# Kernel tuning notes

Measured on AMD Instinct MI355X. Metric: run time of the kernel, lower is better.

The kernel has to match this reference:

```python
import jax, jax.numpy as jnp
import numpy as np
from jax import lax

N, E, DIN, D, L, H, T, NE = 20000, 240000, 768, 256, 3, 4, 9, 8  # nodes, edges, input_dim, gnn_dim, layers, heads, tags, n_etype
DH = D // H
BN_EPS = 1e-5

def _bn(x, g, b):
    # eval-mode BatchNorm1d with running stats (mean=0, var=1)
    return x * (g / np.sqrt(1.0 + BN_EPS)) + b

def _gelu(x):
    return jax.nn.gelu(x, approximate=False)

def setup_inputs():
    key = jax.random.key(0)
    ks = iter(jax.random.split(key, 48))
    nrm = lambda shape: jax.random.normal(next(ks), shape, jnp.float32) * 0.02
    return {
        "node_emb": jax.random.normal(next(ks), (N, DIN), jnp.float32),
        "edge_index": jax.random.randint(next(ks), (2, E), 0, N),
        "edge_type": jax.random.randint(next(ks), (E,), 0, NE),
        "tag_gt": jax.random.randint(next(ks), (N,), 0, T),
        "W_lm2gnn": nrm((DIN, D)), "b_lm2gnn": jnp.zeros((D,)),
        "We1": nrm((L, NE + 1, D)), "be1": jnp.zeros((L, D)),
        "g1": jnp.ones((L, D)), "bb1": jnp.zeros((L, D)),
        "We2": nrm((L, D, D)), "be2": jnp.zeros((L, D)),
        "Wq": nrm((L, D, D)), "bq": jnp.zeros((L, D)),
        "Wk": nrm((L, 2 * D, D)), "bk": jnp.zeros((L, D)),
        "Wm": nrm((L, 2 * D, D)), "bm": jnp.zeros((L, D)),
        "Wp1": nrm((L, D, D)), "bp1": jnp.zeros((L, D)),
        "g2": jnp.ones((L, D)), "bb2": jnp.zeros((L, D)),
        "Wp2": nrm((L, D, D)), "bp2": jnp.zeros((L, D)),
        "Wo": nrm((D, D)), "bo": jnp.zeros((D,)),
        "Wc": nrm((D, D)), "bc": jnp.zeros((D,)),
        "Wt": nrm((D, T)), "bt": jnp.zeros((T,)),
        "crf_start": nrm((T,)), "crf_end": nrm((T,)), "crf_trans": nrm((T, T)),
    }

def _emissions(node_emb, edge_index, edge_type, W_lm2gnn, b_lm2gnn, We1, be1, g1, bb1,
               We2, be2, Wq, bq, Wk, bk, Wm, bm, Wp1, bp1, g2, bb2, Wp2, bp2,
               Wo, bo, Wc, bc, Wt, bt):
    H0 = _gelu(node_emb @ W_lm2gnn + b_lm2gnn)
    loop = jnp.arange(N)
    src = jnp.concatenate([edge_index[0], loop])          # (Etot,)
    dst = jnp.concatenate([edge_index[1], loop])
    # one-hot edge types + self-loop type NE
    ev = jnp.concatenate([jax.nn.one_hot(edge_type, NE + 1, dtype=jnp.float32),
                          jnp.zeros((N, NE + 1), jnp.float32).at[:, NE].set(1.0)], axis=0)
    deg = jax.ops.segment_sum(jnp.ones_like(src, jnp.float32), src, N)[src]  # src out-degree per edge
    X = H0
    for l in range(L):
        e = _bn(ev @ We1[l] + be1[l], g1[l], bb1[l])
        e = jax.nn.relu(e) @ We2[l] + be2[l]              # edge embeddings (Etot, D)
        x_i, x_j = X[dst], X[src]                          # target, source gathers
        q = (x_j @ Wq[l] + bq[l]).reshape(-1, H, DH)
        k = (x_i @ Wk[l][:D] + e @ Wk[l][D:] + bk[l]).reshape(-1, H, DH)
        m = (x_j @ Wm[l][:D] + e @ Wm[l][D:] + bm[l]).reshape(-1, H, DH)
        s = (q * k).sum(-1) / np.sqrt(DH)                  # (Etot, H)
        smax = jax.ops.segment_max(s, src, N)[src]
        ex = jnp.exp(s - smax)
        den = jax.ops.segment_sum(ex, src, N)[src]
        alpha = ex / (den + 1e-16) * deg[:, None]          # segment softmax over src, degree-scaled
        out_e = (m * alpha[:, :, None]).reshape(-1, D)
        aggr = jax.ops.segment_sum(out_e, dst, N)          # scatter-add to targets
        Xl = _bn(aggr @ Wp1[l] + bp1[l], g2[l], bb2[l])
        X = _gelu(jax.nn.relu(Xl) @ Wp2[l] + bp2[l])       # mlp then activation (dropout = eval identity)
    hidden = _gelu((H0 @ Wo + bo) + (X @ Wc + bc))
    return hidden @ Wt + bt                                # (N, T)

def reference(node_emb, edge_index, edge_type, tag_gt, W_lm2gnn, b_lm2gnn, We1, be1, g1, bb1,
              We2, be2, Wq, bq, Wk, bk, Wm, bm, Wp1, bp1, g2, bb2, Wp2, bp2,
              Wo, bo, Wc, bc, Wt, bt, crf_start, crf_end, crf_trans):
    em = _emissions(node_emb, edge_index, edge_type, W_lm2gnn, b_lm2gnn, We1, be1, g1, bb1,
                    We2, be2, Wq, bq, Wk, bk, Wm, bm, Wp1, bp1, g2, bb2, Wp2, bp2,
                    Wo, bo, Wc, bc, Wt, bt)
    # CRF Viterbi decode (batch=1, full-length mask)
    def vstep(score, em_t):
        cand = score[:, None] + crf_trans                  # (T, T)
        return jnp.max(cand, axis=0) + em_t, jnp.argmax(cand, axis=0)
    last, bps = lax.scan(vstep, crf_start + em[0], em[1:])
    last_tag = jnp.argmax(last + crf_end)
    def back(t, bp_t):
        prev = bp_t[t]
        return prev, prev
    _, prevs = lax.scan(back, last_tag, bps, reverse=True)
    path = jnp.concatenate([prevs, last_tag[None]])
    return path[None, :]                                   # (1, N) best tag sequence
```

## Files before the change

kernel.cpp:

```cpp
#include <hip/hip_runtime.h>

#define NN 20000
#define EE 240000
#define ETOTAL 260000
#define DIN 768
#define DD 256
#define NT 9

typedef __attribute__((ext_vector_type(2))) float f32x2;

__device__ __forceinline__ unsigned fenc(float x) {
  unsigned u = __float_as_uint(x);
  return (u & 0x80000000u) ? ~u : (u | 0x80000000u);
}
__device__ __forceinline__ float fdec(unsigned e) {
  unsigned u = (e & 0x80000000u) ? (e ^ 0x80000000u) : ~e;
  return __uint_as_float(u);
}
__device__ __forceinline__ float gelu_f(float x) {
  return 0.5f * x * (1.0f + erff(x * 0.70710678118654752440f));
}

#define VSTEP_CORE(EIN, SIN, SOUT)                                        \
  asm volatile(                                                           \
    "s_nop 2\n\t"                                                         \
    "v_readlane_b32 s84, %[sv], 0\n\t"                                    \
    "v_readlane_b32 s85, %[sv], 1\n\t"                                    \
    "v_readlane_b32 s86, %[sv], 2\n\t"                                    \
    "v_readlane_b32 s87, %[sv], 3\n\t"                                    \
    "v_readlane_b32 s88, %[sv], 4\n\t"                                    \
    "v_readlane_b32 s89, %[sv], 5\n\t"                                    \
    "v_readlane_b32 s90, %[sv], 6\n\t"                                    \
    "v_readlane_b32 s91, %[sv], 7\n\t"                                    \
    "v_readlane_b32 s92, %[sv], 8\n\t"                                    \
    "v_pk_add_f32 v[80:81], s[84:85], %[u01]\n\t"                         \
    "v_pk_add_f32 v[82:83], s[86:87], %[u23]\n\t"                         \
    "v_pk_add_f32 v[84:85], s[88:89], %[u45]\n\t"                         \
    "v_pk_add_f32 v[86:87], s[90:91], %[u67]\n\t"                         \
    "v_add_f32 v88, s92, %[u8]\n\t"                                       \
    "v_max3_f32 v80, v80, v81, v82\n\t"                                   \
    "v_max3_f32 v83, v83, v84, v85\n\t"                                   \
    "v_max3_f32 v86, v86, v87, v88\n\t"                                   \
    "v_max3_f32 v80, v80, v83, v86\n\t"                                   \
    "v_add_f32 %[out], v80, %[e]\n\t"                                     \
    : [out]"=v"(SOUT)                                                     \
    : [sv]"v"(SIN), [e]"v"(EIN),                                          \
      [u01]"v"(tc01), [u23]"v"(tc23), [u45]"v"(tc45), [u67]"v"(tc67),     \
      [u8]"v"(tcol8)                                                      \
    : "s84","s85","s86","s87","s88","s89","s90","s91","s92",              \
      "v80","v81","v82","v83","v84","v85","v86","v87","v88")

#define RUN8(E0, E1) do {                                                 \
  float s0, s1, s2, s3, s4, s5, s6, s7;                                   \
  VSTEP_CORE((E0).x, s, s0); VSTEP_CORE((E0).y, s0, s1);                  \
  VSTEP_CORE((E0).z, s1, s2); VSTEP_CORE((E0).w, s2, s3);                 \
  float4 stq0; stq0.x = s0; stq0.y = s1; stq0.z = s2; stq0.w = s3;        \
  *(float4*)svp = stq0;                                                   \
  VSTEP_CORE((E1).x, s3, s4); VSTEP_CORE((E1).y, s4, s5);                 \
  VSTEP_CORE((E1).z, s5, s6); VSTEP_CORE((E1).w, s6, s7);                 \
  float4 stq1; stq1.x = s4; stq1.y = s5; stq1.z = s6; stq1.w = s7;        \
  *(float4*)(svp + 256) = stq1;                                           \
  s = s7; svp += 512;                                                     \
} while (0)

__global__ __launch_bounds__(256) void gemm_k(
    const float* __restrict__ A, const float* __restrict__ B,
    const float* __restrict__ bias,
    const float* __restrict__ bng, const float* __restrict__ bnb,
    float* __restrict__ C, int M, int K, int N, int act)
{
  __shared__ float As[32][64];
  __shared__ float Bs[32][64];
  const int tid = threadIdx.x;
  const int tx = tid & 15, ty = tid >> 4;
  const int m0 = blockIdx.y * 64, n0 = blockIdx.x * 64;
  float acc[4][4];
#pragma unroll
  for (int i = 0; i < 4; ++i)
#pragma unroll
    for (int j = 0; j < 4; ++j) acc[i][j] = 0.f;

  for (int kk = 0; kk < K; kk += 32) {
#pragma unroll
    for (int L = tid; L < 512; L += 256) {
      int r = L >> 3, c4 = L & 7;
      int gm = m0 + r;
      float4 v = make_float4(0.f, 0.f, 0.f, 0.f);
      if (gm < M) v = *(const float4*)(A + (size_t)gm * K + kk + c4 * 4);
      As[c4 * 4 + 0][r] = v.x; As[c4 * 4 + 1][r] = v.y;
      As[c4 * 4 + 2][r] = v.z; As[c4 * 4 + 3][r] = v.w;
    }
#pragma unroll
    for (int L = tid; L < 512; L += 256) {
      int r = L >> 4, c4 = L & 15;
      *(float4*)&Bs[r][c4 * 4] = *(const float4*)(B + (size_t)(kk + r) * N + n0 + c4 * 4);
    }
    __syncthreads();
#pragma unroll
    for (int k = 0; k < 32; ++k) {
      float a[4], b[4];
      *(float4*)a = *(const float4*)&As[k][ty * 4];
      *(float4*)b = *(const float4*)&Bs[k][tx * 4];
#pragma unroll
      for (int i = 0; i < 4; ++i)
#pragma unroll
        for (int j = 0; j < 4; ++j) acc[i][j] += a[i] * b[j];
    }
    __syncthreads();
  }
  const float bnc = 0.99999500003749968752f;
#pragma unroll
  for (int i = 0; i < 4; ++i) {
    int gm = m0 + ty * 4 + i;
    if (gm >= M) continue;
    float o[4];
#pragma unroll
    for (int j = 0; j < 4; ++j) {
      int n = n0 + tx * 4 + j;
      float x = acc[i][j];
      if (bias) x += bias[n];
      if (act == 1) x = gelu_f(x);
      else if (act == 2) { x = x * (bng[n] * bnc) + bnb[n]; x = fmaxf(x, 0.f); }
      o[j] = x;
    }
    *(float4*)(C + (size_t)gm * N + n0 + tx * 4) = *(const float4*)o;
  }
}

__global__ __launch_bounds__(256) void gemm3_k(
    const float* __restrict__ A, const float* __restrict__ B0,
    const float* __restrict__ bias0, const float* __restrict__ B1,
    const float* __restrict__ B2, float* __restrict__ C0,
    float* __restrict__ C1, float* __restrict__ C2, int M)
{
  __shared__ float As[32][64];
  __shared__ float Bs[3][32][64];
  const int tid = threadIdx.x;
  const int tx = tid & 15, ty = tid >> 4;
  const int m0 = blockIdx.y * 64, n0 = blockIdx.x * 64;
  float acc0[4][4], acc1[4][4], acc2[4][4];
#pragma unroll
  for (int i = 0; i < 4; ++i)
#pragma unroll
    for (int j = 0; j < 4; ++j) { acc0[i][j] = 0.f; acc1[i][j] = 0.f; acc2[i][j] = 0.f; }

  for (int kk = 0; kk < DD; kk += 32) {
#pragma unroll
    for (int L = tid; L < 512; L += 256) {
      int r = L >> 3, c4 = L & 7;
      int gm = m0 + r;
      float4 v = make_float4(0.f, 0.f, 0.f, 0.f);
      if (gm < M) v = *(const float4*)(A + (size_t)gm * DD + kk + c4 * 4);
      As[c4 * 4 + 0][r] = v.x; As[c4 * 4 + 1][r] = v.y;
      As[c4 * 4 + 2][r] = v.z; As[c4 * 4 + 3][r] = v.w;
    }
#pragma unroll
    for (int L = tid; L < 1536; L += 256) {
      int which = L >> 9, r = (L >> 4) & 31, c4 = L & 15;
      const float* Bp = (which == 0) ? B0 : (which == 1) ? B1 : B2;
      *(float4*)&Bs[which][r][c4 * 4] =
          *(const float4*)(Bp + (size_t)(kk + r) * DD + n0 + c4 * 4);
    }
    __syncthreads();
#pragma unroll
    for (int k = 0; k < 32; ++k) {
      float a[4], b0[4], b1[4], b2[4];
      *(float4*)a = *(const float4*)&As[k][ty * 4];
      *(float4*)b0 = *(const float4*)&Bs[0][k][tx * 4];
      *(float4*)b1 = *(const float4*)&Bs[1][k][tx * 4];
      *(float4*)b2 = *(const float4*)&Bs[2][k][tx * 4];
#pragma unroll
      for (int i = 0; i < 4; ++i)
#pragma unroll
        for (int j = 0; j < 4; ++j) {
          acc0[i][j] += a[i] * b0[j];
          acc1[i][j] += a[i] * b1[j];
          acc2[i][j] += a[i] * b2[j];
        }
    }
    __syncthreads();
  }
#pragma unroll
  for (int i = 0; i < 4; ++i) {
    int gm = m0 + ty * 4 + i;
    if (gm >= M) continue;
    float o0[4], o1[4], o2[4];
#pragma unroll
    for (int j = 0; j < 4; ++j) {
      int n = n0 + tx * 4 + j;
      o0[j] = acc0[i][j] + bias0[n];
      o1[j] = acc1[i][j];
      o2[j] = acc2[i][j];
    }
    *(float4*)(C0 + (size_t)gm * DD + n0 + tx * 4) = *(const float4*)o0;
    *(float4*)(C1 + (size_t)gm * DD + n0 + tx * 4) = *(const float4*)o1;
    *(float4*)(C2 + (size_t)gm * DD + n0 + tx * 4) = *(const float4*)o2;
  }
}

__global__ __launch_bounds__(256) void gemm_cat_k(
    const float* __restrict__ A1, const float* __restrict__ B1,
    const float* __restrict__ bias1, const float* __restrict__ A2,
    const float* __restrict__ B2, const float* __restrict__ bias2,
    float* __restrict__ C, int M)
{
  __shared__ float As[32][64];
  __shared__ float Bs[32][64];
  const int tid = threadIdx.x;
  const int tx = tid & 15, ty = tid >> 4;
  const int m0 = blockIdx.y * 64, n0 = blockIdx.x * 64;
  float acc[4][4];
#pragma unroll
  for (int i = 0; i < 4; ++i)
#pragma unroll
    for (int j = 0; j < 4; ++j) acc[i][j] = 0.f;

  for (int kk = 0; kk < 2 * DD; kk += 32) {
    const float* Ap = (kk < DD) ? A1 : A2;
    const float* Bp = (kk < DD) ? B1 : B2;
    const int ko = kk & (DD - 1);
#pragma unroll
    for (int L = tid; L < 512; L += 256) {
      int r = L >> 3, c4 = L & 7;
      int gm = m0 + r;
      float4 v = make_float4(0.f, 0.f, 0.f, 0.f);
      if (gm < M) v = *(const float4*)(Ap + (size_t)gm * DD + ko + c4 * 4);
      As[c4 * 4 + 0][r] = v.x; As[c4 * 4 + 1][r] = v.y;
      As[c4 * 4 + 2][r] = v.z; As[c4 * 4 + 3][r] = v.w;
    }
#pragma unroll
    for (int L = tid; L < 512; L += 256) {
      int r = L >> 4, c4 = L & 15;
      *(float4*)&Bs[r][c4 * 4] = *(const float4*)(Bp + (size_t)(ko + r) * DD + n0 + c4 * 4);
    }
    __syncthreads();
#pragma unroll
    for (int k = 0; k < 32; ++k) {
      float a[4], b[4];
      *(float4*)a = *(const float4*)&As[k][ty * 4];
      *(float4*)b = *(const float4*)&Bs[k][tx * 4];
#pragma unroll
      for (int i = 0; i < 4; ++i)
#pragma unroll
        for (int j = 0; j < 4; ++j) acc[i][j] += a[i] * b[j];
    }
    __syncthreads();
  }
#pragma unroll
  for (int i = 0; i < 4; ++i) {
    int gm = m0 + ty * 4 + i;
    if (gm >= M) continue;
    float o[4];
#pragma unroll
    for (int j = 0; j < 4; ++j) {
      int n = n0 + tx * 4 + j;
      o[j] = gelu_f(acc[i][j] + bias1[n] + bias2[n]);
    }
    *(float4*)(C + (size_t)gm * DD + n0 + tx * 4) = *(const float4*)o;
  }
}

__global__ __launch_bounds__(256) void edge_tables_k(
    const float* __restrict__ We1l, const float* __restrict__ be1l,
    const float* __restrict__ g1l, const float* __restrict__ bb1l,
    const float* __restrict__ We2l, const float* __restrict__ be2l,
    const float* __restrict__ WkEl, const float* __restrict__ bkl,
    const float* __restrict__ WmEl, const float* __restrict__ bml,
    float* __restrict__ ketab, float* __restrict__ metab)
{
  __shared__ float r_s[DD];
  __shared__ float e_s[DD];
  const int t = blockIdx.x, d = threadIdx.x;
  const float bnc = 0.99999500003749968752f;
  float pre = We1l[t * DD + d] + be1l[d];
  float bnv = pre * (g1l[d] * bnc) + bb1l[d];
  r_s[d] = fmaxf(bnv, 0.f);
  __syncthreads();
  float acc = 0.f;
  for (int c = 0; c < DD; ++c) acc += r_s[c] * We2l[c * DD + d];
  e_s[d] = acc + be2l[d];
  __syncthreads();
  float ka = 0.f, ma = 0.f;
  for (int c = 0; c < DD; ++c) {
    float ec = e_s[c];
    ka += ec * WkEl[c * DD + d];
    ma += ec * WmEl[c * DD + d];
  }
  ketab[t * DD + d] = ka + bkl[d];
  metab[t * DD + d] = ma + bml[d];
}

__global__ void deg_k(const int* __restrict__ ei, int* __restrict__ cnt,
                      int* __restrict__ cnt_d)
{
  for (int e = blockIdx.x * blockDim.x + threadIdx.x; e < EE; e += gridDim.x * blockDim.x) {
    atomicAdd(&cnt[ei[e]], 1);
    atomicAdd(&cnt_d[ei[EE + e]], 1);
  }
}

__global__ __launch_bounds__(256) void scan_k(const int* __restrict__ c,
                                              int* __restrict__ offs)
{
  __shared__ int part[257];
  const int tid = threadIdx.x;
  const int CH = (NN + 255) / 256;
  int a = tid * CH, b = a + CH; if (b > NN) b = NN;
  int s = 0;
  for (int i = a; i < b; ++i) s += c[i];
  part[tid] = s;
  __syncthreads();
  if (tid == 0) {
    int r = 0;
    for (int i = 0; i < 256; ++i) { int v = part[i]; part[i] = r; r += v; }
    part[256] = r;
  }
  __syncthreads();
  int r = part[tid];
  for (int i = a; i < b; ++i) { offs[i] = r; r += c[i]; }
  if (tid == 255) offs[NN] = part[256];
}

__global__ void fill_k(const int* __restrict__ ei, const int* __restrict__ offs,
                       int* __restrict__ fc, int* __restrict__ eix)
{
  for (int e = blockIdx.x * blockDim.x + threadIdx.x; e < EE; e += gridDim.x * blockDim.x) {
    int d = ei[EE + e];
    int p = offs[d] + atomicAdd(&fc[d], 1);
    eix[p] = e;
  }
}

__global__ __launch_bounds__(256) void score_k(
    const float* __restrict__ Q, const float* __restrict__ Kn,
    const float* __restrict__ ketab, const int* __restrict__ ei,
    const int* __restrict__ et, float* __restrict__ sbuf,
    unsigned* __restrict__ smax)
{
  __shared__ float ke_s[NT * DD];
  for (int i = threadIdx.x; i < NT * DD; i += 256) ke_s[i] = ketab[i];
  __syncthreads();
  const int lane = threadIdx.x & 63, wave = threadIdx.x >> 6;
  const float4* Q4 = (const float4*)Q;
  const float4* K4 = (const float4*)Kn;
  for (int e = blockIdx.x * 4 + wave; e < ETOTAL; e += gridDim.x * 4) {
    int src, dst, t;
    if (e < EE) { src = ei[e]; dst = ei[EE + e]; t = et[e]; }
    else { src = dst = e - EE; t = NT - 1; }
    float4 q = Q4[src * 64 + lane];
    float4 k = K4[dst * 64 + lane];
    float4 ke = *(const float4*)(ke_s + t * DD + lane * 4);
    float p = q.x * (k.x + ke.x) + q.y * (k.y + ke.y) +
              q.z * (k.z + ke.z) + q.w * (k.w + ke.w);
    p += __shfl_xor(p, 8); p += __shfl_xor(p, 4);
    p += __shfl_xor(p, 2); p += __shfl_xor(p, 1);
    if ((lane & 15) == 0) {
      int h = lane >> 4;
      float s = p * 0.125f;
      sbuf[e * 4 + h] = s;
      atomicMax(smax + src * 4 + h, fenc(s));
    }
  }
}

__global__ void softmax_k(const int* __restrict__ ei, float* __restrict__ sbuf,
                          const unsigned* __restrict__ smax, float* __restrict__ den)
{
  for (int idx = blockIdx.x * blockDim.x + threadIdx.x; idx < ETOTAL * 4;
       idx += gridDim.x * blockDim.x) {
    int e = idx >> 2, h = idx & 3;
    int src = (e < EE) ? ei[e] : e - EE;
    float s = sbuf[idx];
    float ex = expf(s - fdec(smax[src * 4 + h]));
    sbuf[idx] = ex;
    atomicAdd(den + src * 4 + h, ex);
  }
}

__global__ __launch_bounds__(256) void aggr2_k(
    const float* __restrict__ Mn, const float* __restrict__ metab,
    const int* __restrict__ ei, const int* __restrict__ et,
    const float* __restrict__ sbuf, const float* __restrict__ den,
    const int* __restrict__ cnt, const int* __restrict__ offs,
    const int* __restrict__ eix, float* __restrict__ aggr)
{
  __shared__ float me_s[NT * DD];
  for (int i = threadIdx.x; i < NT * DD; i += 256) me_s[i] = metab[i];
  __syncthreads();
  const int lane = threadIdx.x & 63, wave = threadIdx.x >> 6;
  const int h = lane >> 4;
  const float4* M4 = (const float4*)Mn;
  int dst = blockIdx.x * 4 + wave;
  if (dst >= NN) return;
  float4 acc;
  {
    float ex = sbuf[(EE + dst) * 4 + h];
    float dn = den[dst * 4 + h];
    float alpha = ex / (dn + 1e-16f) * (float)(cnt[dst] + 1);
    float4 m = M4[dst * 64 + lane];
    float4 me = *(const float4*)(me_s + (NT - 1) * DD + lane * 4);
    acc.x = (m.x + me.x) * alpha; acc.y = (m.y + me.y) * alpha;
    acc.z = (m.z + me.z) * alpha; acc.w = (m.w + me.w) * alpha;
  }
  int o1 = offs[dst + 1];
  for (int o = offs[dst]; o < o1; ++o) {
    int e = eix[o];
    int src = ei[e], t = et[e];
    float ex = sbuf[e * 4 + h];
    float dn = den[src * 4 + h];
    float alpha = ex / (dn + 1e-16f) * (float)(cnt[src] + 1);
    float4 m = M4[src * 64 + lane];
    float4 me = *(const float4*)(me_s + t * DD + lane * 4);
    acc.x += (m.x + me.x) * alpha; acc.y += (m.y + me.y) * alpha;
    acc.z += (m.z + me.z) * alpha; acc.w += (m.w + me.w) * alpha;
  }
  ((float4*)aggr)[dst * 64 + lane] = acc;
}

__global__ __launch_bounds__(256) void emis_k(
    const float* __restrict__ hidden, const float* __restrict__ Wt,
    const float* __restrict__ bt, float* __restrict__ em)
{
  __shared__ float wt_s[DD * NT];
  for (int i = threadIdx.x; i < DD * NT; i += 256) wt_s[i] = Wt[i];
  __syncthreads();
  const int lane = threadIdx.x & 63, wave = threadIdx.x >> 6;
  const float4* H4 = (const float4*)hidden;
  for (int n = blockIdx.x * 4 + wave; n < NN; n += gridDim.x * 4) {
    float4 h = H4[n * 64 + lane];
    const float* w0 = wt_s + (lane * 4) * NT;
    float p[NT];
#pragma unroll
    for (int t = 0; t < NT; ++t)
      p[t] = h.x * w0[t] + h.y * w0[NT + t] + h.z * w0[2 * NT + t] + h.w * w0[3 * NT + t];
#pragma unroll
    for (int m = 32; m >= 1; m >>= 1)
#pragma unroll
      for (int t = 0; t < NT; ++t) p[t] += __shfl_xor(p[t], m);
    if (lane == 0) {
#pragma unroll
      for (int t = 0; t < NT; ++t) em[n * NT + t] = p[t] + bt[t];
    }
  }
}

__global__ __launch_bounds__(256) void viterbi_k(
    const float* __restrict__ em, const float* __restrict__ cstart,
    const float* __restrict__ cend, const float* __restrict__ ctrans,
    float* __restrict__ sv, int* __restrict__ outp)
{
  const int VCS = 512;
  const int ST = VCS + 12;
  const int NCH = (NN + VCS - 1) / VCS;
  __shared__ float embufT[2][NT][VCS + 12];
  __shared__ float trT[NT * 16];
  __shared__ float scf[NT];
  __shared__ unsigned char fmaps[256][NT];
  __shared__ unsigned char ends_s[256];
  __shared__ int last_s;
  const int tid = threadIdx.x, lane = tid & 63, wave = tid >> 6;
  const int jl = min(lane & 15, NT - 1);

  for (int i = tid; i < VCS * NT; i += 256) {
    int t = i / NT, j = i - t * NT;
    embufT[0][j][t] = em[i];
  }
  if (tid < NT * NT) trT[(tid % NT) * 16 + (tid / NT)] = ctrans[tid];
  __syncthreads();

  f32x2 tc01, tc23, tc45, tc67;
  float tcol8 = 0.f;
  float s = 0.f;
  if (wave == 0) {
    tc01[0] = ctrans[0 * NT + jl]; tc01[1] = ctrans[1 * NT + jl];
    tc23[0] = ctrans[2 * NT + jl]; tc23[1] = ctrans[3 * NT + jl];
    tc45[0] = ctrans[4 * NT + jl]; tc45[1] = ctrans[5 * NT + jl];
    tc67[0] = ctrans[6 * NT + jl]; tc67[1] = ctrans[7 * NT + jl];
    tcol8   = ctrans[8 * NT + jl];
    s = cstart[jl] + embufT[0][jl][0];
    sv[lane * 4] = s;
  }

  for (int c = 0; c < NCH; ++c) {
    if (wave > 0) {
      if (c + 1 < NCH) {
        int base = (c + 1) * VCS * NT;
        int n2 = VCS * NT;
        if (base + n2 > NN * NT) n2 = NN * NT - base;
        float* dstb = &embufT[(c + 1) & 1][0][0];
        for (int i = tid - 64; i < n2; i += 192) {
          int t = i / NT, j = i - t * NT;
          dstb[j * ST + t] = em[base + i];
        }
      }
    } else {
      const float* ebT = &embufT[c & 1][0][0] + (size_t)jl * ST;
      int tbeg = (c == 0) ? 1 : c * VCS;
      int tend = (c + 1) * VCS; if (tend > NN) tend = NN;
      int off = tbeg - c * VCS;
      int nsteps = tend - tbeg;
      int pre = (8 - (tbeg & 7)) & 7; if (pre > nsteps) pre = nsteps;
      for (int i = 0; i < pre; ++i) {
        int t = tbeg + i;
        float e0 = ebT[off + i];
        float so;
        VSTEP_CORE(e0, s, so);
        s = so;
        sv[((size_t)t >> 2) * 256 + lane * 4 + (t & 3)] = s;
      }
      int rem = nsteps - pre;
      int ngr = rem >> 3;
      int tof = off + pre;
      float* svp = sv + ((size_t)(tbeg + pre) >> 2) * 256 + lane * 4;
      if (ngr > 0) {
        float4 eA0 = *(const float4*)&ebT[tof];
        float4 eA1 = *(const float4*)&ebT[tof + 4];
        float4 eB0, eB1;
        int g = 0;
        while (g + 2 <= ngr) {
          eB0 = *(const float4*)&ebT[tof + (g + 1) * 8];
          eB1 = *(const float4*)&ebT[tof + (g + 1) * 8 + 4];
          RUN8(eA0, eA1);
          eA0 = *(const float4*)&ebT[tof + (g + 2) * 8];
          eA1 = *(const float4*)&ebT[tof + (g + 2) * 8 + 4];
          RUN8(eB0, eB1);
          g += 2;
        }
        if (g < ngr) RUN8(eA0, eA1);
      }
      for (int i = pre + (ngr << 3); i < nsteps; ++i) {
        int t = tbeg + i;
        float e0 = ebT[off + i];
        float so;
        VSTEP_CORE(e0, s, so);
        s = so;
        sv[((size_t)t >> 2) * 256 + lane * 4 + (t & 3)] = s;
      }
    }
    __syncthreads();
  }

  if (wave == 0 && lane < NT) scf[lane] = s + cend[lane];
  __syncthreads();
  if (tid == 0) {
    float bv = scf[0]; int bi = 0;
    for (int j = 1; j < NT; ++j) if (scf[j] > bv) { bv = scf[j]; bi = j; }
    last_s = bi;
  }
  __syncthreads();

  const int RL = 79;
  int a = 1 + tid * RL;
  int b = a + RL; if (b > NN) b = NN;
  bool active = (a < NN);
  if (active) {
    int x[NT];
#pragma unroll
    for (int j = 0; j < NT; ++j) x[j] = j;
    for (int t = b - 1; t >= a; --t) {
      const float* sp = sv + ((size_t)(t - 1) >> 2) * 256 + ((t - 1) & 3);
      float sr[NT];
#pragma unroll
      for (int i = 0; i < NT; ++i) sr[i] = sp[i * 4];
#pragma unroll
      for (int j = 0; j < NT; ++j) {
        const float* tcx = trT + x[j] * 16;
        float bv = sr[0] + tcx[0]; int bi = 0;
#pragma unroll
        for (int i = 1; i < NT; ++i) {
          float cv = sr[i] + tcx[i];
          if (cv > bv) { bv = cv; bi = i; }
        }
        x[j] = bi;
      }
    }
#pragma unroll
    for (int j = 0; j < NT; ++j) fmaps[tid][j] = (unsigned char)x[j];
  }
  __syncthreads();
  if (tid == 0) {
    int x = last_s;
    for (int k = 255; k >= 0; --k) {
      ends_s[k] = (unsigned char)x;
      int ak = 1 + k * RL;
      if (ak < NN) x = fmaps[k][x];
    }
  }
  __syncthreads();
  if (active) {
    int x = ends_s[tid];
    outp[b - 1] = x;
    for (int t = b - 1; t >= a; --t) {
      const float* sp = sv + ((size_t)(t - 1) >> 2) * 256 + ((t - 1) & 3);
      const float* tcx = trT + x * 16;
      float bv = sp[0] + tcx[0]; int bi = 0;
#pragma unroll
      for (int i = 1; i < NT; ++i) {
        float cv = sp[i * 4] + tcx[i];
        if (cv > bv) { bv = cv; bi = i; }
      }
      x = bi;
      outp[t - 1] = x;
    }
  }
}

extern "C" void kernel_launch(void* const* d_in, const int* in_sizes, int n_in,
                              void* d_out, int out_size, void* d_ws, size_t ws_size,
                              hipStream_t stream)
{
  const float* node_emb = (const float*)d_in[0];
  const int* edge_index = (const int*)d_in[1];
  const int* edge_type = (const int*)d_in[2];
  const float* W_lm2gnn = (const float*)d_in[4];
  const float* b_lm2gnn = (const float*)d_in[5];
  const float* We1 = (const float*)d_in[6];
  const float* be1 = (const float*)d_in[7];
  const float* g1 = (const float*)d_in[8];
  const float* bb1 = (const float*)d_in[9];
  const float* We2 = (const float*)d_in[10];
  const float* be2 = (const float*)d_in[11];
  const float* Wq = (const float*)d_in[12];
  const float* bq = (const float*)d_in[13];
  const float* Wk = (const float*)d_in[14];
  const float* bk = (const float*)d_in[15];
  const float* Wm = (const float*)d_in[16];
  const float* bm = (const float*)d_in[17];
  const float* Wp1 = (const float*)d_in[18];
  const float* bp1 = (const float*)d_in[19];
  const float* g2 = (const float*)d_in[20];
  const float* bb2 = (const float*)d_in[21];
  const float* Wp2 = (const float*)d_in[22];
  const float* bp2 = (const float*)d_in[23];
  const float* Wo = (const float*)d_in[24];
  const float* bo = (const float*)d_in[25];
  const float* Wc = (const float*)d_in[26];
  const float* bc = (const float*)d_in[27];
  const float* Wt = (const float*)d_in[28];
  const float* bt = (const float*)d_in[29];
  const float* cstart = (const float*)d_in[30];
  const float* cend = (const float*)d_in[31];
  const float* ctrans = (const float*)d_in[32];

  const size_t NB = (size_t)NN * DD * sizeof(float);
  char* w = (char*)d_ws;
  float* H0 = (float*)(w + 0 * NB);
  float* Xb = (float*)(w + 1 * NB);
  float* Qb = (float*)(w + 2 * NB);
  float* Kb = (float*)(w + 3 * NB);
  float* Mb = (float*)(w + 4 * NB);
  char* sm = w + 5 * NB;
  size_t smo = 0;
  auto alloc = [&](size_t bytes) { char* p = sm + smo; smo += (bytes + 255) & ~255ull; return p; };
  float* sbuf = (float*)alloc((size_t)ETOTAL * 4 * 4);
  unsigned* smax = (unsigned*)alloc((size_t)NN * 4 * 4);
  float* den = (float*)alloc((size_t)NN * 4 * 4);
  int* cnt = (int*)alloc((size_t)NN * 4);
  int* cnt_d = (int*)alloc((size_t)NN * 4);
  int* offs = (int*)alloc((size_t)(NN + 1) * 4);
  int* fc = (int*)alloc((size_t)NN * 4);
  int* eix = (int*)alloc((size_t)EE * 4);
  float* ketab = (float*)alloc((size_t)NT * DD * 4);
  float* metab = (float*)alloc((size_t)NT * DD * 4);
  float* em = (float*)alloc((size_t)NN * NT * 4);
  float* sv = (float*)alloc(((size_t)NN * 64 + 256) * 4);
  const size_t needed = 5 * NB + smo;
  if (ws_size < needed) return;

  dim3 gg(DD / 64, (NN + 63) / 64);

  hipMemsetAsync(cnt, 0, (size_t)((char*)eix - (char*)cnt), stream);
  deg_k<<<1024, 256, 0, stream>>>(edge_index, cnt, cnt_d);
  scan_k<<<1, 256, 0, stream>>>(cnt_d, offs);
  fill_k<<<1024, 256, 0, stream>>>(edge_index, offs, fc, eix);

  gemm_k<<<gg, 256, 0, stream>>>(node_emb, W_lm2gnn, b_lm2gnn, nullptr,
                                 nullptr, H0, NN, DIN, DD, 1);

  const float* Xcur = H0;
  for (int l = 0; l < 3; ++l) {
    edge_tables_k<<<NT, 256, 0, stream>>>(
        We1 + (size_t)l * NT * DD, be1 + l * DD, g1 + l * DD, bb1 + l * DD,
        We2 + (size_t)l * DD * DD, be2 + l * DD,
        Wk + (size_t)l * 2 * DD * DD + DD * DD, bk + l * DD,
        Wm + (size_t)l * 2 * DD * DD + DD * DD, bm + l * DD, ketab, metab);

    gemm3_k<<<gg, 256, 0, stream>>>(Xcur, Wq + (size_t)l * DD * DD, bq + l * DD,
                                    Wk + (size_t)l * 2 * DD * DD,
                                    Wm + (size_t)l * 2 * DD * DD,
                                    Qb, Kb, Mb, NN);

    hipMemsetAsync(smax, 0, (size_t)NN * 4 * 4 * 2, stream);
    score_k<<<2048, 256, 0, stream>>>(Qb, Kb, ketab, edge_index, edge_type, sbuf, smax);
    softmax_k<<<2048, 256, 0, stream>>>(edge_index, sbuf, smax, den);

    aggr2_k<<<(NN + 3) / 4, 256, 0, stream>>>(Mb, metab, edge_index, edge_type,
                                              sbuf, den, cnt, offs, eix, Kb);

    gemm_k<<<gg, 256, 0, stream>>>(Kb, Wp1 + (size_t)l * DD * DD, bp1 + l * DD,
                                   g2 + l * DD, bb2 + l * DD, Qb, NN, DD, DD, 2);
    gemm_k<<<gg, 256, 0, stream>>>(Qb, Wp2 + (size_t)l * DD * DD, bp2 + l * DD,
                                   nullptr, nullptr, Xb, NN, DD, DD, 1);
    Xcur = Xb;
  }

  gemm_cat_k<<<gg, 256, 0, stream>>>(H0, Wo, bo, Xb, Wc, bc, Qb, NN);

  emis_k<<<1250, 256, 0, stream>>>(Qb, Wt, bt, em);
  viterbi_k<<<1, 256, 0, stream>>>(em, cstart, cend, ctrans, sv, (int*)d_out);
}
```

Baseline: 2.719 ms.

## Replace atomic edge softmax with source-sorted CSR segmented softmax

Builds a second CSR index grouped by source node and computes each node's per-head softmax max and denominator with one wave per node using shuffle reductions. This replaces the atomicMax/atomicAdd scatter kernels and the per-layer memset. The exponential is now recomputed inside the aggregation kernel from the stored max and sum. The cost is an extra scan and fill pass at setup, plus more expf work and a float2 load in aggregation.

```diff
diff --git a/kernel.cpp b/kernel.cpp
--- a/kernel.cpp
+++ b/kernel.cpp
@@ -9,14 +9,6 @@
 
 typedef __attribute__((ext_vector_type(2))) float f32x2;
 
-__device__ __forceinline__ unsigned fenc(float x) {
-  unsigned u = __float_as_uint(x);
-  return (u & 0x80000000u) ? ~u : (u | 0x80000000u);
-}
-__device__ __forceinline__ float fdec(unsigned e) {
-  unsigned u = (e & 0x80000000u) ? (e ^ 0x80000000u) : ~e;
-  return __uint_as_float(u);
-}
 __device__ __forceinline__ float gelu_f(float x) {
   return 0.5f * x * (1.0f + erff(x * 0.70710678118654752440f));
 }
@@ -321,11 +313,11 @@
   if (tid == 255) offs[NN] = part[256];
 }
 
-__global__ void fill_k(const int* __restrict__ ei, const int* __restrict__ offs,
+__global__ void fill_k(const int* __restrict__ key, const int* __restrict__ offs,
                        int* __restrict__ fc, int* __restrict__ eix)
 {
   for (int e = blockIdx.x * blockDim.x + threadIdx.x; e < EE; e += gridDim.x * blockDim.x) {
-    int d = ei[EE + e];
+    int d = key[e];
     int p = offs[d] + atomicAdd(&fc[d], 1);
     eix[p] = e;
   }
@@ -334,8 +326,7 @@
 __global__ __launch_bounds__(256) void score_k(
     const float* __restrict__ Q, const float* __restrict__ Kn,
     const float* __restrict__ ketab, const int* __restrict__ ei,
-    const int* __restrict__ et, float* __restrict__ sbuf,
-    unsigned* __restrict__ smax)
+    const int* __restrict__ et, float* __restrict__ sbuf)
 {
   __shared__ float ke_s[NT * DD];
   for (int i = threadIdx.x; i < NT * DD; i += 256) ke_s[i] = ketab[i];
@@ -356,31 +347,42 @@
     p += __shfl_xor(p, 2); p += __shfl_xor(p, 1);
     if ((lane & 15) == 0) {
       int h = lane >> 4;
-      float s = p * 0.125f;
-      sbuf[e * 4 + h] = s;
-      atomicMax(smax + src * 4 + h, fenc(s));
-    }
-  }
-}
-
-__global__ void softmax_k(const int* __restrict__ ei, float* __restrict__ sbuf,
-                          const unsigned* __restrict__ smax, float* __restrict__ den)
-{
-  for (int idx = blockIdx.x * blockDim.x + threadIdx.x; idx < ETOTAL * 4;
-       idx += gridDim.x * blockDim.x) {
-    int e = idx >> 2, h = idx & 3;
-    int src = (e < EE) ? ei[e] : e - EE;
-    float s = sbuf[idx];
-    float ex = expf(s - fdec(smax[src * 4 + h]));
-    sbuf[idx] = ex;
-    atomicAdd(den + src * 4 + h, ex);
-  }
+      sbuf[e * 4 + h] = p * 0.125f;
+    }
+  }
+}
+
+__global__ __launch_bounds__(256) void smx_k(
+    const float* __restrict__ sbuf, const int* __restrict__ offs_s,
+    const int* __restrict__ eix_s, float2* __restrict__ sd)
+{
+  const int lane = threadIdx.x & 63, wave = threadIdx.x >> 6;
+  const int h = lane >> 4, sl = lane & 15;
+  int src = blockIdx.x * 4 + wave;
+  if (src >= NN) return;
+  int o0 = offs_s[src], o1 = offs_s[src + 1];
+  float sself = sbuf[(EE + src) * 4 + h];
+  float mx = (sl == 0) ? sself : -__builtin_inff();
+  for (int o = o0 + sl; o < o1; o += 16) {
+    int e = eix_s[o];
+    mx = fmaxf(mx, sbuf[e * 4 + h]);
+  }
+#pragma unroll
+  for (int m = 8; m >= 1; m >>= 1) mx = fmaxf(mx, __shfl_xor(mx, m));
+  float sum = (sl == 0) ? expf(sself - mx) : 0.f;
+  for (int o = o0 + sl; o < o1; o += 16) {
+    int e = eix_s[o];
+    sum += expf(sbuf[e * 4 + h] - mx);
+  }
+#pragma unroll
+  for (int m = 8; m >= 1; m >>= 1) sum += __shfl_xor(sum, m);
+  if (sl == 0) sd[src * 4 + h] = make_float2(mx, sum);
 }
 
 __global__ __launch_bounds__(256) void aggr2_k(
     const float* __restrict__ Mn, const float* __restrict__ metab,
     const int* __restrict__ ei, const int* __restrict__ et,
-    const float* __restrict__ sbuf, const float* __restrict__ den,
+    const float* __restrict__ sbuf, const float2* __restrict__ sd,
     const int* __restrict__ cnt, const int* __restrict__ offs,
     const int* __restrict__ eix, float* __restrict__ aggr)
 {
@@ -394,9 +396,9 @@
   if (dst >= NN) return;
   float4 acc;
   {
-    float ex = sbuf[(EE + dst) * 4 + h];
-    float dn = den[dst * 4 + h];
-    float alpha = ex / (dn + 1e-16f) * (float)(cnt[dst] + 1);
+    float2 sdv = sd[dst * 4 + h];
+    float ex = expf(sbuf[(EE + dst) * 4 + h] - sdv.x);
+    float alpha = ex / (sdv.y + 1e-16f) * (float)(cnt[dst] + 1);
     float4 m = M4[dst * 64 + lane];
     float4 me = *(const float4*)(me_s + (NT - 1) * DD + lane * 4);
     acc.x = (m.x + me.x) * alpha; acc.y = (m.y + me.y) * alpha;
@@ -406,9 +408,9 @@
   for (int o = offs[dst]; o < o1; ++o) {
     int e = eix[o];
     int src = ei[e], t = et[e];
-    float ex = sbuf[e * 4 + h];
-    float dn = den[src * 4 + h];
-    float alpha = ex / (dn + 1e-16f) * (float)(cnt[src] + 1);
+    float2 sdv = sd[src * 4 + h];
+    float ex = expf(sbuf[e * 4 + h] - sdv.x);
+    float alpha = ex / (sdv.y + 1e-16f) * (float)(cnt[src] + 1);
     float4 m = M4[src * 64 + lane];
     float4 me = *(const float4*)(me_s + t * DD + lane * 4);
     acc.x += (m.x + me.x) * alpha; acc.y += (m.y + me.y) * alpha;
@@ -653,13 +655,15 @@
   size_t smo = 0;
   auto alloc = [&](size_t bytes) { char* p = sm + smo; smo += (bytes + 255) & ~255ull; return p; };
   float* sbuf = (float*)alloc((size_t)ETOTAL * 4 * 4);
-  unsigned* smax = (unsigned*)alloc((size_t)NN * 4 * 4);
-  float* den = (float*)alloc((size_t)NN * 4 * 4);
   int* cnt = (int*)alloc((size_t)NN * 4);
   int* cnt_d = (int*)alloc((size_t)NN * 4);
   int* offs = (int*)alloc((size_t)(NN + 1) * 4);
   int* fc = (int*)alloc((size_t)NN * 4);
+  int* offs_s = (int*)alloc((size_t)(NN + 1) * 4);
+  int* fc_s = (int*)alloc((size_t)NN * 4);
   int* eix = (int*)alloc((size_t)EE * 4);
+  int* eix_s = (int*)alloc((size_t)EE * 4);
+  float2* sd = (float2*)alloc((size_t)NN * 4 * 8);
   float* ketab = (float*)alloc((size_t)NT * DD * 4);
   float* metab = (float*)alloc((size_t)NT * DD * 4);
   float* em = (float*)alloc((size_t)NN * NT * 4);
@@ -672,7 +676,9 @@
   hipMemsetAsync(cnt, 0, (size_t)((char*)eix - (char*)cnt), stream);
   deg_k<<<1024, 256, 0, stream>>>(edge_index, cnt, cnt_d);
   scan_k<<<1, 256, 0, stream>>>(cnt_d, offs);
-  fill_k<<<1024, 256, 0, stream>>>(edge_index, offs, fc, eix);
+  scan_k<<<1, 256, 0, stream>>>(cnt, offs_s);
+  fill_k<<<1024, 256, 0, stream>>>(edge_index + EE, offs, fc, eix);
+  fill_k<<<1024, 256, 0, stream>>>(edge_index, offs_s, fc_s, eix_s);
 
   gemm_k<<<gg, 256, 0, stream>>>(node_emb, W_lm2gnn, b_lm2gnn, nullptr,
                                  nullptr, H0, NN, DIN, DD, 1);
@@ -690,12 +696,11 @@
                                     Wm + (size_t)l * 2 * DD * DD,
                                     Qb, Kb, Mb, NN);
 
-    hipMemsetAsync(smax, 0, (size_t)NN * 4 * 4 * 2, stream);
-    score_k<<<2048, 256, 0, stream>>>(Qb, Kb, ketab, edge_index, edge_type, sbuf, smax);
-    softmax_k<<<2048, 256, 0, stream>>>(edge_index, sbuf, smax, den);
+    score_k<<<2048, 256, 0, stream>>>(Qb, Kb, ketab, edge_index, edge_type, sbuf);
+    smx_k<<<(NN + 3) / 4, 256, 0, stream>>>(sbuf, offs_s, eix_s, sd);
 
     aggr2_k<<<(NN + 3) / 4, 256, 0, stream>>>(Mb, metab, edge_index, edge_type,
-                                              sbuf, den, cnt, offs, eix, Kb);
+                                              sbuf, sd, cnt, offs, eix, Kb);
 
     gemm_k<<<gg, 256, 0, stream>>>(Kb, Wp1 + (size_t)l * DD * DD, bp1 + l * DD,
                                    g2 + l * DD, bb2 + l * DD, Qb, NN, DD, DD, 2);
```

Measured after the change: 2.741 ms. No clear change (+0.8%).
